# Performance work log

Measured on AMD Instinct MI355X. Metric: run time of the kernel, lower is better.

The kernel has to match this reference:

```python
import jax, jax.numpy as jnp
import numpy as np

B, N1, N2 = 4, 16384, 4096   # scenes, fine points/scene, coarse points/scene
CIN, COUT = 512, 256
K = 3
EPS_BN = 1e-5
EPS_D = 1e-8


def setup_inputs() -> dict:
    key = jax.random.key(0)
    ks = jax.random.split(key, 6)
    return {
        "point_1": jax.random.uniform(ks[0], (B * N1, 3), dtype=jnp.float32),
        "feat_1": jax.random.normal(ks[1], (B * N1, COUT), dtype=jnp.float32) * 0.1,
        "point_2": jax.random.uniform(ks[2], (B * N2, 3), dtype=jnp.float32),
        "feat_2": jax.random.normal(ks[3], (B * N2, CIN), dtype=jnp.float32) * 0.1,
        "W1": jax.random.normal(ks[4], (COUT, COUT), dtype=jnp.float32) / np.sqrt(COUT).astype(np.float32),
        "b1": jnp.zeros((COUT,), jnp.float32),
        "g1": jnp.ones((COUT,), jnp.float32),
        "beta1": jnp.zeros((COUT,), jnp.float32),
        "W2": jax.random.normal(ks[5], (CIN, COUT), dtype=jnp.float32) / np.sqrt(CIN).astype(np.float32),
        "b2": jnp.zeros((COUT,), jnp.float32),
        "g2": jnp.ones((COUT,), jnp.float32),
        "beta2": jnp.zeros((COUT,), jnp.float32),
        # equal-sized segments: row_splits = [0, N, 2N, ...]
        "row_splits_1": jnp.arange(B + 1, dtype=jnp.int32) * N1,
        "row_splits_2": jnp.arange(B + 1, dtype=jnp.int32) * N2,
    }


def _bn(x, gamma, beta):
    # BatchNorm1d, training mode (biased variance, as in torch)
    mu = x.mean(0)
    var = x.var(0)
    return gamma * (x - mu) * jax.lax.rsqrt(var + EPS_BN) + beta


def reference(point_1, feat_1, point_2, feat_2,
              W1, b1, g1, beta1, W2, b2, g2, beta2,
              row_splits_1, row_splits_2):
    # linear1(feat_1): Linear + BN + ReLU
    f1 = jax.nn.relu(_bn(feat_1 @ W1 + b1, g1, beta1))          # [B*N1, COUT]
    # linear2(feat_2): Linear + BN + ReLU
    f2 = jax.nn.relu(_bn(feat_2 @ W2 + b2, g2, beta2))          # [B*N2, COUT]

    # batched KNN (equal row_splits -> reshape into [B, n, 3])
    q = point_1.reshape(B, N1, 3)
    p = point_2.reshape(B, N2, 3)
    d2 = ((q * q).sum(-1)[:, :, None]
          + (p * p).sum(-1)[:, None, :]
          - 2.0 * jnp.einsum("bnd,bmd->bnm", q, p))             # [B, N1, N2] squared dists
    neg_d, idx = jax.lax.top_k(-d2, K)                           # [B, N1, K]
    dist = jnp.maximum(-neg_d, 0.0)

    # inverse-distance weights (knn search is non-differentiable in the original)
    recip = 1.0 / (dist + EPS_D)
    w = jax.lax.stop_gradient(recip / recip.sum(-1, keepdims=True))  # [B, N1, K]

    # gather + weighted sum (three-interpolate)
    f2b = f2.reshape(B, N2, COUT)
    gathered = f2b[jnp.arange(B)[:, None, None], idx]            # [B, N1, K, COUT]
    interp = (gathered * w[..., None]).sum(2).reshape(B * N1, COUT)

    return f1 + interp
```

## Files before the change

kernel.cpp:

```cpp
#include <hip/hip_runtime.h>
#include <hip/hip_bf16.h>
#include <math.h>

#define N1R 65536
#define N2R 16384
#define NPB 4096
#define NQB 16384
#define CC  256
#define NCELL 512
#define GRID_FAIL_R2 0.015625f

typedef __attribute__((ext_vector_type(4))) float v4f;
typedef __attribute__((ext_vector_type(8))) short v8s;

static __device__ __forceinline__ short f2bs(float f) {
    union { __hip_bfloat16 h; short s; } u;
    u.h = __float2bfloat16(f);
    return u.s;
}

static __device__ __forceinline__ int cell_of(float x, float y, float z) {
    const int cx = min(7, (int)(x * 8.0f));
    const int cy = min(7, (int)(y * 8.0f));
    const int cz = min(7, (int)(z * 8.0f));
    return (cz << 6) | (cy << 3) | cx;
}

static __device__ __forceinline__ void ins3(float d, int si,
    float& b0, float& b1, float& b2, int& i0, int& i1, int& i2)
{
    const bool lt0 = (d < b0) | ((d == b0) & (si < i0));
    const bool lt1 = (d < b1) | ((d == b1) & (si < i1));
    const bool lt2 = (d < b2) | ((d == b2) & (si < i2));
    b2 = lt1 ? b1 : (lt2 ? d : b2);   i2 = lt1 ? i1 : (lt2 ? si : i2);
    b1 = lt0 ? b0 : (lt1 ? d : b1);   i1 = lt0 ? i0 : (lt1 ? si : i1);
    b0 = lt0 ? d  : b0;               i0 = lt0 ? si : i0;
}

__global__ __launch_bounds__(256)
void wtrans_kernel(const float* __restrict__ W, short* __restrict__ WT, int Kd)
{
    const int i = blockIdx.x * 256 + threadIdx.x;
    const int k = i >> 8;
    const int n = i & 255;
    WT[(size_t)n * Kd + k] = f2bs(W[i]);
}

__global__ __launch_bounds__(256)
void paug_count_kernel(const float* __restrict__ p2, float4* __restrict__ paug,
                       int* __restrict__ counts_p)
{
#pragma clang fp contract(off)
    const int i = blockIdx.x * 256 + threadIdx.x;
    const float x = p2[(size_t)i * 3 + 0];
    const float y = p2[(size_t)i * 3 + 1];
    const float z = p2[(size_t)i * 3 + 2];
    float4 v;
    v.x = x; v.y = y; v.z = z;
    v.w = (x * x + y * y) + z * z;
    paug[i] = v;
    const int b = i >> 12;
    atomicAdd(&counts_p[b * NCELL + cell_of(x, y, z)], 1);
}

__global__ __launch_bounds__(256)
void qcount_kernel(const float* __restrict__ p1, int* __restrict__ counts_q)
{
    const int i = blockIdx.x * 256 + threadIdx.x;
    const float x = p1[(size_t)i * 3 + 0];
    const float y = p1[(size_t)i * 3 + 1];
    const float z = p1[(size_t)i * 3 + 2];
    const int b = i >> 14;
    atomicAdd(&counts_q[b * NCELL + cell_of(x, y, z)], 1);
}

__global__ __launch_bounds__(512)
void prefix_kernel(const int* __restrict__ counts_p, int* __restrict__ cursors_p,
                   int* __restrict__ starts_p,
                   const int* __restrict__ counts_q, int* __restrict__ cursors_q)
{
    __shared__ int sc[512];
    const int t = threadIdx.x;
    for (int a = 0; a < 8; ++a) {
        const int b = a & 3;
        const int* cnt = (a < 4) ? counts_p + b * NCELL : counts_q + b * NCELL;
        const int v = cnt[t];
        sc[t] = v;
        __syncthreads();
        for (int off = 1; off < 512; off <<= 1) {
            const int add = (t >= off) ? sc[t - off] : 0;
            __syncthreads();
            sc[t] += add;
            __syncthreads();
        }
        const int incl = sc[t];
        const int excl = incl - v;
        if (a < 4) {
            starts_p[b * 513 + t] = excl;
            if (t == 511) starts_p[b * 513 + 512] = incl;
            cursors_p[b * NCELL + t] = excl;
        } else {
            cursors_q[b * NCELL + t] = excl;
        }
        __syncthreads();
    }
}

__global__ __launch_bounds__(256)
void scatter_p_kernel(const float4* __restrict__ paug, int* __restrict__ cursors,
                      float4* __restrict__ sortedP, unsigned short* __restrict__ sIdx)
{
    const int i = blockIdx.x * 256 + threadIdx.x;
    const float4 v = paug[i];
    const int b = i >> 12;
    const int cell = cell_of(v.x, v.y, v.z);
    const int pos = atomicAdd(&cursors[b * NCELL + cell], 1);
    sortedP[(size_t)b * NPB + pos] = v;
    sIdx[(size_t)b * NPB + pos] = (unsigned short)(i & 4095);
}

__global__ __launch_bounds__(256)
void scatter_q_kernel(const float* __restrict__ p1, int* __restrict__ cursors,
                      unsigned short* __restrict__ qlist)
{
    const int i = blockIdx.x * 256 + threadIdx.x;
    const float x = p1[(size_t)i * 3 + 0];
    const float y = p1[(size_t)i * 3 + 1];
    const float z = p1[(size_t)i * 3 + 2];
    const int b = i >> 14;
    const int cell = cell_of(x, y, z);
    const int pos = atomicAdd(&cursors[b * NCELL + cell], 1);
    qlist[(size_t)b * NQB + pos] = (unsigned short)(i & 16383);
}

template<int KD>
__global__ __launch_bounds__(256)
void gemm_fused_kernel(const float* __restrict__ X,
                       const short* __restrict__ WT,
                       const float* __restrict__ bias,
                       float* __restrict__ Y,
                       float* __restrict__ sum, float* __restrict__ sumsq)
{
    const int bm0 = blockIdx.x * 128;
    const int bn0 = blockIdx.y * 128;
    const int wave = threadIdx.x >> 6;
    const int lane = threadIdx.x & 63;
    const int wm0 = (wave >> 1) * 64;
    const int wn0 = (wave & 1) * 64;
    const int col = lane & 15, quad = lane >> 4;

    v4f acc[4][4];
#pragma unroll
    for (int i = 0; i < 4; ++i)
#pragma unroll
        for (int j = 0; j < 4; ++j) acc[i][j] = (v4f){0.f, 0.f, 0.f, 0.f};

    const short* wbase = WT + (size_t)(bn0 + wn0 + col) * KD + quad * 8;
    const float* xbase = X + (size_t)(bm0 + wm0 + col) * KD + quad * 8;

#pragma unroll 2
    for (int k0 = 0; k0 < KD; k0 += 32) {
        v8s bf[4];
#pragma unroll
        for (int ni = 0; ni < 4; ++ni)
            bf[ni] = *(const v8s*)(wbase + (size_t)(ni * 16) * KD + k0);

        v8s a[4];
#pragma unroll
        for (int mi = 0; mi < 4; ++mi) {
            const float* xp = xbase + (size_t)(mi * 16) * KD + k0;
            const v4f p = *(const v4f*)xp;
            const v4f q = *(const v4f*)(xp + 4);
            v8s t;
#pragma unroll
            for (int j = 0; j < 4; ++j) { t[j] = f2bs(p[j]); t[j + 4] = f2bs(q[j]); }
            a[mi] = t;
        }

#pragma unroll
        for (int mi = 0; mi < 4; ++mi)
#pragma unroll
            for (int ni = 0; ni < 4; ++ni)
                acc[mi][ni] = __builtin_amdgcn_mfma_f32_16x16x32_bf16(a[mi], bf[ni], acc[mi][ni], 0, 0, 0);
    }

#pragma unroll
    for (int ni = 0; ni < 4; ++ni) {
        const int n = bn0 + wn0 + ni * 16 + col;
        const float bv = bias[n];
        float s = 0.f, q = 0.f;
#pragma unroll
        for (int mi = 0; mi < 4; ++mi) {
            const int m = bm0 + wm0 + mi * 16 + quad * 4;
#pragma unroll
            for (int r = 0; r < 4; ++r) {
                const float y = acc[mi][ni][r] + bv;
                Y[(size_t)(m + r) * CC + n] = y;
                s += y; q += y * y;
            }
        }
        s += __shfl_xor(s, 16); q += __shfl_xor(q, 16);
        s += __shfl_xor(s, 32); q += __shfl_xor(q, 32);
        if (quad == 0) { atomicAdd(&sum[n], s); atomicAdd(&sumsq[n], q); }
    }
}

__global__ __launch_bounds__(512)
void finalize_kernel(const float* __restrict__ sums,
                     const float* __restrict__ g1, const float* __restrict__ be1,
                     const float* __restrict__ g2, const float* __restrict__ be2,
                     float* __restrict__ ac)
{
    const int t = threadIdx.x;
    const int c = t & 255;
    const int which = t >> 8;
    const float* s = sums + which * 512;
    const double n = which ? (double)N2R : (double)N1R;
    const double mu = (double)s[c] / n;
    const double var = (double)s[c + 256] / n - mu * mu;
    const float g  = which ? g2[c]  : g1[c];
    const float be = which ? be2[c] : be1[c];
    const double a  = (double)g / sqrt(var + 1e-5);
    const double cv = (double)be - a * mu;
    ac[which * 512 + c]       = (float)a;
    ac[which * 512 + 256 + c] = (float)cv;
}

__global__ __launch_bounds__(256)
void knn_grid_kernel(const float* __restrict__ p1,
                     const float4* __restrict__ sortedP,
                     const unsigned short* __restrict__ sIdx16,
                     const int* __restrict__ starts_p,
                     const unsigned short* __restrict__ qlist,
                     int* __restrict__ idx_out, float* __restrict__ w_out,
                     int* __restrict__ failCount, int* __restrict__ failList)
{
#pragma clang fp contract(off)
    __shared__ float4 sP[NPB];
    __shared__ unsigned short sI[NPB];
    __shared__ int sS[513];
    __shared__ float mD[128 * 3];
    __shared__ int   mI[128 * 3];

    const int b = blockIdx.x >> 7;
    const int slot0 = (blockIdx.x & 127) * 128;
    const int tid = threadIdx.x;
    const int lq = tid & 127;
    const int half = tid >> 7;

    {
        const float4* gp = sortedP + (size_t)b * NPB;
        for (int i = tid; i < NPB; i += 256) sP[i] = gp[i];
        const unsigned int* gi = (const unsigned int*)(sIdx16 + (size_t)b * NPB);
        unsigned int* li = (unsigned int*)sI;
        for (int i = tid; i < NPB / 2; i += 256) li[i] = gi[i];
        const int* gs = starts_p + b * 513;
        for (int i = tid; i < 513; i += 256) sS[i] = gs[i];
    }

    const int q = qlist[(size_t)b * NQB + slot0 + lq];
    const int qid = b * NQB + q;
    const float qx = p1[(size_t)qid * 3 + 0];
    const float qy = p1[(size_t)qid * 3 + 1];
    const float qz = p1[(size_t)qid * 3 + 2];
    const float qq = (qx * qx + qy * qy) + qz * qz;
    const int cqx = min(7, (int)(qx * 8.0f));
    const int cqy = min(7, (int)(qy * 8.0f));
    const int cqz = min(7, (int)(qz * 8.0f));

    __syncthreads();

    float b0 = 3.0e38f, b1 = 3.0e38f, b2 = 3.0e38f;
    int i0 = 0x7fffffff, i1 = 0x7fffffff, i2 = 0x7fffffff;

    int n = 0;
    for (int dz = -1; dz <= 1; ++dz)
        for (int dy = -1; dy <= 1; ++dy)
            for (int dx = -1; dx <= 1; ++dx, ++n) {
                if (half ? (n < 14) : (n >= 14)) continue;
                const int cz = cqz + dz, cy = cqy + dy, cx = cqx + dx;
                if (((unsigned)cz | (unsigned)cy | (unsigned)cx) > 7u) continue;
                const int cell = (cz << 6) | (cy << 3) | cx;
                const int ks = sS[cell], ke = sS[cell + 1];
                for (int k = ks; k < ke; ++k) {
                    const float4 P = sP[k];
                    const int si = sI[k];
                    const float dot = fmaf(qz, P.z, fmaf(qy, P.y, qx * P.x));
                    const float d = fmaf(-2.0f, dot, qq + P.w);
                    ins3(d, si, b0, b1, b2, i0, i1, i2);
                }
            }

    if (half) {
        mD[lq * 3 + 0] = b0; mD[lq * 3 + 1] = b1; mD[lq * 3 + 2] = b2;
        mI[lq * 3 + 0] = i0; mI[lq * 3 + 1] = i1; mI[lq * 3 + 2] = i2;
    }
    __syncthreads();
    if (!half) {
#pragma unroll
        for (int r = 0; r < 3; ++r)
            ins3(mD[lq * 3 + r], mI[lq * 3 + r], b0, b1, b2, i0, i1, i2);

        if (!(b2 < GRID_FAIL_R2)) {
            const int p = atomicAdd(failCount, 1);
            if (p < N1R) failList[p] = qid;
        }
        const float r0 = 1.0f / (fmaxf(b0, 0.0f) + 1e-8f);
        const float r1 = 1.0f / (fmaxf(b1, 0.0f) + 1e-8f);
        const float r2 = 1.0f / (fmaxf(b2, 0.0f) + 1e-8f);
        const float rs = (r0 + r1) + r2;
        idx_out[(size_t)qid * 3 + 0] = i0;
        idx_out[(size_t)qid * 3 + 1] = i1;
        idx_out[(size_t)qid * 3 + 2] = i2;
        w_out[(size_t)qid * 3 + 0] = r0 / rs;
        w_out[(size_t)qid * 3 + 1] = r1 / rs;
        w_out[(size_t)qid * 3 + 2] = r2 / rs;
    }
}

__global__ __launch_bounds__(256)
void knn_bf_kernel(const float* __restrict__ p1,
                   const float4* __restrict__ paug,
                   const int* __restrict__ failCount,
                   const int* __restrict__ failList,
                   int* __restrict__ idx_out, float* __restrict__ w_out)
{
#pragma clang fp contract(off)
    const int nf = min(*failCount, N1R);
    const int gw = (blockIdx.x * 256 + threadIdx.x) >> 6;
    const int lane = threadIdx.x & 63;
    const int nw = (gridDim.x * 256) >> 6;

    for (int fi = gw; fi < nf; fi += nw) {
        const int qid = failList[fi];
        const int b = qid >> 14;
        const float qx = p1[(size_t)qid * 3 + 0];
        const float qy = p1[(size_t)qid * 3 + 1];
        const float qz = p1[(size_t)qid * 3 + 2];
        const float qq = (qx * qx + qy * qy) + qz * qz;

        float b0 = 3.0e38f, b1 = 3.0e38f, b2 = 3.0e38f;
        int i0 = 0x7fffffff, i1 = 0x7fffffff, i2 = 0x7fffffff;

        const float4* pb = paug + (size_t)b * NPB;
        for (int j = lane; j < NPB; j += 64) {
            const float4 P = pb[j];
            const float dot = fmaf(qz, P.z, fmaf(qy, P.y, qx * P.x));
            const float d = fmaf(-2.0f, dot, qq + P.w);
            ins3(d, j, b0, b1, b2, i0, i1, i2);
        }
        for (int m = 1; m < 64; m <<= 1) {
            const float c0 = __shfl_xor(b0, m), c1 = __shfl_xor(b1, m), c2 = __shfl_xor(b2, m);
            const int j0 = __shfl_xor(i0, m), j1 = __shfl_xor(i1, m), j2 = __shfl_xor(i2, m);
            ins3(c0, j0, b0, b1, b2, i0, i1, i2);
            ins3(c1, j1, b0, b1, b2, i0, i1, i2);
            ins3(c2, j2, b0, b1, b2, i0, i1, i2);
        }
        if (lane == 0) {
            const float r0 = 1.0f / (fmaxf(b0, 0.0f) + 1e-8f);
            const float r1 = 1.0f / (fmaxf(b1, 0.0f) + 1e-8f);
            const float r2 = 1.0f / (fmaxf(b2, 0.0f) + 1e-8f);
            const float rs = (r0 + r1) + r2;
            idx_out[(size_t)qid * 3 + 0] = i0;
            idx_out[(size_t)qid * 3 + 1] = i1;
            idx_out[(size_t)qid * 3 + 2] = i2;
            w_out[(size_t)qid * 3 + 0] = r0 / rs;
            w_out[(size_t)qid * 3 + 1] = r1 / rs;
            w_out[(size_t)qid * 3 + 2] = r2 / rs;
        }
    }
}

__global__ __launch_bounds__(256)
void final_kernel(float* __restrict__ Y1out,
                  const float* __restrict__ Y2raw,
                  const float* __restrict__ ac,
                  const int* __restrict__ idx, const float* __restrict__ w)
{
    const int r = blockIdx.x * 4 + (threadIdx.x >> 6);
    const int cg = threadIdx.x & 63;
    const int b = r >> 14;

    v4f a1 = *(const v4f*)(ac + cg * 4);
    v4f c1 = *(const v4f*)(ac + 256 + cg * 4);
    v4f a2 = *(const v4f*)(ac + 512 + cg * 4);
    v4f c2 = *(const v4f*)(ac + 768 + cg * 4);
    v4f y = *(const v4f*)(Y1out + (size_t)r * CC + cg * 4);
    v4f s;
#pragma unroll
    for (int j = 0; j < 4; ++j)
        s[j] = fmaxf(fmaf(a1[j], y[j], c1[j]), 0.f);

    const int*   ir = idx + (size_t)r * 3;
    const float* wr = w   + (size_t)r * 3;
#pragma unroll
    for (int k = 0; k < 3; ++k) {
        const int id = ir[k];
        const float wk = wr[k];
        v4f g = *(const v4f*)(Y2raw + ((size_t)(b * NPB + id)) * CC + cg * 4);
#pragma unroll
        for (int j = 0; j < 4; ++j) {
            const float gv = fmaxf(fmaf(a2[j], g[j], c2[j]), 0.f);
            s[j] = fmaf(wk, gv, s[j]);
        }
    }
    *(v4f*)(Y1out + (size_t)r * CC + cg * 4) = s;
}

extern "C" void kernel_launch(void* const* d_in, const int* in_sizes, int n_in,
                              void* d_out, int out_size, void* d_ws, size_t ws_size,
                              hipStream_t stream)
{
    const float* point1 = (const float*)d_in[0];
    const float* feat1  = (const float*)d_in[1];
    const float* point2 = (const float*)d_in[2];
    const float* feat2  = (const float*)d_in[3];
    const float* W1     = (const float*)d_in[4];
    const float* b1     = (const float*)d_in[5];
    const float* g1     = (const float*)d_in[6];
    const float* beta1  = (const float*)d_in[7];
    const float* W2     = (const float*)d_in[8];
    const float* b2     = (const float*)d_in[9];
    const float* g2     = (const float*)d_in[10];
    const float* beta2  = (const float*)d_in[11];

    float* Y1 = (float*)d_out;

    char* ws = (char*)d_ws;
    float*          Y2       = (float*)ws;
    float*          stats    = (float*)(ws + (size_t)16777216);
    int*            counts_p = (int*)  (ws + (size_t)16781312);
    int*            counts_q = (int*)  (ws + (size_t)16789504);
    int*            failCnt  = (int*)  (ws + (size_t)16797696);
    int*            cursors_p= (int*)  (ws + (size_t)16801792);
    int*            cursors_q= (int*)  (ws + (size_t)16809984);
    int*            starts_p = (int*)  (ws + (size_t)16818176);
    float*          ac       = (float*)(ws + (size_t)16826624);
    unsigned short* sIdx16   = (unsigned short*)(ws + (size_t)16830720);
    unsigned short* qlist    = (unsigned short*)(ws + (size_t)16863488);
    int*            failList = (int*)  (ws + (size_t)16994560);
    float4*         sortedP  = (float4*)(ws + (size_t)17256704);
    int*            idxb     = (int*)  (ws + (size_t)17518848);
    float*          wb       = (float*)(ws + (size_t)18305280);
    short*          WT1      = (short*)(ws + (size_t)19091712);
    short*          WT2      = (short*)(ws + (size_t)19222784);
    float4*         paug     = (float4*)(ws + (size_t)19484928);

    hipMemsetAsync(stats, 0, 24576, stream);

    wtrans_kernel<<<256, 256, 0, stream>>>(W1, WT1, 256);
    wtrans_kernel<<<512, 256, 0, stream>>>(W2, WT2, 512);

    paug_count_kernel<<<N2R / 256, 256, 0, stream>>>(point2, paug, counts_p);
    qcount_kernel<<<N1R / 256, 256, 0, stream>>>(point1, counts_q);
    prefix_kernel<<<1, 512, 0, stream>>>(counts_p, cursors_p, starts_p, counts_q, cursors_q);
    scatter_p_kernel<<<N2R / 256, 256, 0, stream>>>(paug, cursors_p, sortedP, sIdx16);
    scatter_q_kernel<<<N1R / 256, 256, 0, stream>>>(point1, cursors_q, qlist);

    gemm_fused_kernel<256><<<dim3(N1R / 128, 2), 256, 0, stream>>>(feat1, WT1, b1, Y1,
                                                                   stats + 0,   stats + 256);
    gemm_fused_kernel<512><<<dim3(N2R / 128, 2), 256, 0, stream>>>(feat2, WT2, b2, Y2,
                                                                   stats + 512, stats + 768);

    finalize_kernel<<<1, 512, 0, stream>>>(stats, g1, beta1, g2, beta2, ac);

    knn_grid_kernel<<<512, 256, 0, stream>>>(point1, sortedP, sIdx16, starts_p,
                                             qlist, idxb, wb, failCnt, failList);
    knn_bf_kernel<<<256, 256, 0, stream>>>(point1, paug, failCnt, failList, idxb, wb);

    final_kernel<<<N1R / 4, 256, 0, stream>>>(Y1, Y2, ac, idxb, wb);
}
```

Before: 365.3 us.

## Stage bf16-converted A tile in shared memory with register prefetch in GEMM

The GEMM now loads each 128x32 slice of X cooperatively, converts it to bf16 once, and stores it to an LDS tile that the waves read for their MFMA A operands. Before, each wave loaded and converted its own rows, so every A element was fetched and converted by both N-waves. The next slice is prefetched into registers while the current one is consumed. In exchange it adds two barriers per k-step, and the compile-time K template becomes a runtime argument, which may weaken unrolling.

```diff
diff --git a/kernel.cpp b/kernel.cpp
--- a/kernel.cpp
+++ b/kernel.cpp
@@ -7,6 +7,7 @@
 #define NPB 4096
 #define NQB 16384
 #define CC  256
+#define ASTRIDE 40
 #define NCELL 512
 #define GRID_FAIL_R2 0.015625f
 
@@ -133,14 +134,16 @@
     qlist[(size_t)b * NQB + pos] = (unsigned short)(i & 16383);
 }
 
-template<int KD>
 __global__ __launch_bounds__(256)
 void gemm_fused_kernel(const float* __restrict__ X,
                        const short* __restrict__ WT,
                        const float* __restrict__ bias,
                        float* __restrict__ Y,
-                       float* __restrict__ sum, float* __restrict__ sumsq)
-{
+                       float* __restrict__ sum, float* __restrict__ sumsq,
+                       int Kdim)
+{
+    __shared__ short As[128 * ASTRIDE];
+
     const int bm0 = blockIdx.x * 128;
     const int bn0 = blockIdx.y * 128;
     const int wave = threadIdx.x >> 6;
@@ -149,34 +152,53 @@
     const int wn0 = (wave & 1) * 64;
     const int col = lane & 15, quad = lane >> 4;
 
+    const int srow = threadIdx.x >> 1;
+    const int skh  = (threadIdx.x & 1) * 16;
+    const float* sbase = X + (size_t)(bm0 + srow) * Kdim + skh;
+    short* sdst = As + srow * ASTRIDE + skh;
+
     v4f acc[4][4];
 #pragma unroll
     for (int i = 0; i < 4; ++i)
 #pragma unroll
         for (int j = 0; j < 4; ++j) acc[i][j] = (v4f){0.f, 0.f, 0.f, 0.f};
 
-    const short* wbase = WT + (size_t)(bn0 + wn0 + col) * KD + quad * 8;
-    const float* xbase = X + (size_t)(bm0 + wm0 + col) * KD + quad * 8;
-
-#pragma unroll 2
-    for (int k0 = 0; k0 < KD; k0 += 32) {
+    const short* wbase = WT + (size_t)(bn0 + wn0 + col) * Kdim + quad * 8;
+
+    v4f f0 = *(const v4f*)(sbase);
+    v4f f1 = *(const v4f*)(sbase + 4);
+    v4f f2v = *(const v4f*)(sbase + 8);
+    v4f f3 = *(const v4f*)(sbase + 12);
+
+    for (int k0 = 0; k0 < Kdim; k0 += 32) {
+        v8s lo, hi;
+#pragma unroll
+        for (int j = 0; j < 4; ++j) {
+            lo[j] = f2bs(f0[j]); lo[j + 4] = f2bs(f1[j]);
+            hi[j] = f2bs(f2v[j]); hi[j + 4] = f2bs(f3[j]);
+        }
+        __syncthreads();
+        *(v8s*)sdst = lo;
+        *(v8s*)(sdst + 8) = hi;
+        __syncthreads();
+
         v8s bf[4];
 #pragma unroll
         for (int ni = 0; ni < 4; ++ni)
-            bf[ni] = *(const v8s*)(wbase + (size_t)(ni * 16) * KD + k0);
+            bf[ni] = *(const v8s*)(wbase + (size_t)(ni * 16) * Kdim + k0);
+
+        if (k0 + 32 < Kdim) {
+            const float* np = sbase + k0 + 32;
+            f0 = *(const v4f*)np;
+            f1 = *(const v4f*)(np + 4);
+            f2v = *(const v4f*)(np + 8);
+            f3 = *(const v4f*)(np + 12);
+        }
 
         v8s a[4];
 #pragma unroll
-        for (int mi = 0; mi < 4; ++mi) {
-            const float* xp = xbase + (size_t)(mi * 16) * KD + k0;
-            const v4f p = *(const v4f*)xp;
-            const v4f q = *(const v4f*)(xp + 4);
-            v8s t;
-#pragma unroll
-            for (int j = 0; j < 4; ++j) { t[j] = f2bs(p[j]); t[j + 4] = f2bs(q[j]); }
-            a[mi] = t;
-        }
-
+        for (int mi = 0; mi < 4; ++mi)
+            a[mi] = *(const v8s*)(As + (wm0 + mi * 16 + col) * ASTRIDE + quad * 8);
 #pragma unroll
         for (int mi = 0; mi < 4; ++mi)
 #pragma unroll
@@ -457,10 +479,10 @@
     scatter_p_kernel<<<N2R / 256, 256, 0, stream>>>(paug, cursors_p, sortedP, sIdx16);
     scatter_q_kernel<<<N1R / 256, 256, 0, stream>>>(point1, cursors_q, qlist);
 
-    gemm_fused_kernel<256><<<dim3(N1R / 128, 2), 256, 0, stream>>>(feat1, WT1, b1, Y1,
-                                                                   stats + 0,   stats + 256);
-    gemm_fused_kernel<512><<<dim3(N2R / 128, 2), 256, 0, stream>>>(feat2, WT2, b2, Y2,
-                                                                   stats + 512, stats + 768);
+    gemm_fused_kernel<<<dim3(N1R / 128, 2), 256, 0, stream>>>(feat1, WT1, b1, Y1,
+                                                              stats + 0,   stats + 256, 256);
+    gemm_fused_kernel<<<dim3(N2R / 128, 2), 256, 0, stream>>>(feat2, WT2, b2, Y2,
+                                                              stats + 512, stats + 768, 512);
 
     finalize_kernel<<<1, 512, 0, stream>>>(stats, g1, beta1, g2, beta2, ac);
 
```

Result: faster. 345.5 us (-5.4%).
